# Kernel tuning notes

Hardware: AMD Instinct MI355X
Metric: run time of the kernel (lower is better)

Reference implementation:

```python
import jax, jax.numpy as jnp
import numpy as np
from jax import lax

IN_CHANNELS = 4
STEPS_IN_ITR = 3


def one_step_ltm(x, T):
    # x: [B, H, W]; T: [B, 10, H, W] (9 stencil weight planes + bias plane)
    B, H, W = x.shape
    xp = jnp.pad(x, ((0, 0), (1, 1), (1, 1)))
    out = T[:, 9]
    k = 0
    # original ordering: X0..X2 scan row-offset with col-offset 0, X3..X5 col 1, X6..X8 col 2
    for dj in range(3):
        for di in range(3):
            out = out + xp[:, di:di + H, dj:dj + W] * T[:, k]
            k += 1
    return out


def setup_inputs() -> dict:
    key = jax.random.key(0)
    k1, k2, k3 = jax.random.split(key, 3)
    B, Tt, C, H, W = 8, 16, 1, 512, 512
    x = jax.random.uniform(k1, (B, Tt, C, H, W), dtype=jnp.float32)
    # stand-in unet: 3x3 SAME conv, in_channels -> 10
    W_unet = jax.random.normal(k2, (10, IN_CHANNELS, 3, 3), dtype=jnp.float32) * 0.1
    b_unet = jax.random.normal(k3, (10,), dtype=jnp.float32) * 0.1
    return {"x": x, "W_unet": W_unet, "b_unet": b_unet}


def reference(x, W_unet, b_unet):
    B, Tt, C, H, W = x.shape
    x_in = x[:, -IN_CHANNELS:, 0]  # [B, in_channels, H, W]
    T = lax.conv_general_dilated(
        x_in, W_unet, window_strides=(1, 1), padding='SAME',
        dimension_numbers=('NCHW', 'OIHW', 'NCHW')) + b_unet[None, :, None, None]

    xt0 = one_step_ltm(x[:, -1, 0], T)  # stored at t=0 WITHOUT sigmoid (as in original)

    def body(xt, _):
        for _j in range(STEPS_IN_ITR):
            xt = one_step_ltm(xt, T)
            xt = jax.nn.sigmoid(one_step_ltm(xt, T))
        return xt, xt

    _, xs = lax.scan(body, xt0, None, length=Tt - 1)  # [Tt-1, B, H, W]
    seq = jnp.concatenate([xt0[None], xs], axis=0)     # [Tt, B, H, W]
    seq = jnp.transpose(seq, (1, 0, 2, 3))             # [B, Tt, H, W]
    xout = jnp.zeros((B, Tt, C, H, W), dtype=x.dtype).at[:, :, 0].set(seq)
    return xout
```

## Files before the change

kernel.cpp:

```cpp
#include <hip/hip_runtime.h>
#include <hip/hip_fp16.h>
#include <math.h>

#define Bd 8
#define Td 16
#define Hd 512
#define Wd 512
#define HWc (Hd * Wd)
#define NPIX (Bd * HWc)

#define CT  16
#define CR  18
#define CP  20
#define CTH2 256

#define WCR 128
#define WCC 64
#define WH  6
#define WTR 140
#define WTC 76
#define WLP 77
#define WTHR 1024
#define WRPG 11
#define WNG 13

#define FMAMIX_LO(acc, wv, hv) \
    asm("v_fma_mix_f32 %0, %1, %2, %0 op_sel:[0,0,0] op_sel_hi:[0,1,0]" \
        : "+v"(acc) : "v"(wv), "v"(hv))
#define FMAMIX_HI(acc, wv, hv) \
    asm("v_fma_mix_f32 %0, %1, %2, %0 op_sel:[0,1,0] op_sel_hi:[0,1,0]" \
        : "+v"(acc) : "v"(wv), "v"(hv))

__device__ __forceinline__ float hi_half_f32(unsigned h) {
    __half2 hh = *(__half2*)&h;
    return __half2float(__high2half(hh));
}

__global__ __launch_bounds__(CTH2)
void conv_step0_kernel(const float* __restrict__ x,
                       const float* __restrict__ Wu,
                       const float* __restrict__ bu,
                       __half2* __restrict__ T,
                       float* __restrict__ out) {
    __shared__ float sX[4][CR][CP];

    int bx  = blockIdx.x;
    int b   = bx >> 10;
    int rem = bx & 1023;
    int by  = rem >> 5;
    int bc  = rem & 31;
    int i0  = by * CT;
    int j0  = bc * CT;

    const float* xb = x + ((size_t)b * Td + 12) * HWc;
    int tid = threadIdx.x;

    for (int idx = tid; idx < 4 * CR * CR; idx += CTH2) {
        int ch = idx / (CR * CR);
        int r2 = idx - ch * (CR * CR);
        int r  = r2 / CR;
        int c  = r2 - r * CR;
        int gi = i0 + r - 1, gj = j0 + c - 1;
        float v = 0.0f;
        if ((unsigned)gi < (unsigned)Hd && (unsigned)gj < (unsigned)Wd)
            v = xb[(size_t)ch * HWc + gi * Wd + gj];
        sX[ch][r][c] = v;
    }
    __syncthreads();

    int tx = tid & 15;
    int ty = tid >> 4;

    float xf[36];
    #pragma unroll
    for (int ch = 0; ch < 4; ++ch)
        #pragma unroll
        for (int kh = 0; kh < 3; ++kh)
            #pragma unroll
            for (int kw = 0; kw < 3; ++kw)
                xf[(ch * 3 + kh) * 3 + kw] = sX[ch][ty + kh][tx + kw];

    int gi = i0 + ty;
    int gj = j0 + tx;
    size_t pix = (size_t)gi * Wd + gj;
    __half2* Tb = T + (size_t)b * 5 * HWc;

    float o0 = 0.0f;
    float accPrev = 0.0f;
    #pragma unroll
    for (int o = 0; o < 10; ++o) {
        const float* wo = Wu + o * 36;
        float acc = bu[o];
        #pragma unroll
        for (int z = 0; z < 36; ++z)
            acc += xf[z] * wo[z];

        if (o < 9)
            o0 += xf[(3 * 3 + (o % 3)) * 3 + (o / 3)] * acc;
        else
            o0 += acc;

        if (o & 1) {
            __half2 h = __floats2half2_rn(accPrev, acc);
            *(unsigned*)(Tb + (size_t)(o >> 1) * HWc + pix) = *(unsigned*)&h;
        }
        accPrev = acc;
    }

    out[(size_t)b * Td * HWc + pix] = o0;
}

__global__ __launch_bounds__(WTHR, 2)
void fused6_wide_kernel(const float* __restrict__ xin,
                        const __half2* __restrict__ T,
                        float* __restrict__ xout) {
    __shared__ float sA[WTR * WLP];
    __shared__ float sB[WTR * WLP];

    int tile = blockIdx.x;
    int b  = tile >> 5;
    int tr = (tile >> 3) & 3;
    int tc = tile & 7;
    int ri = tr * WCR - WH;
    int rj = tc * WCC - WH;

    const float* xb = xin + (size_t)b * Td * HWc;
    const __half2* Tb = T + (size_t)b * 5 * HWc;
    float* ob = xout + (size_t)b * Td * HWc;
    int tid = threadIdx.x;

    for (int idx = tid; idx < WTR * WTC; idx += WTHR) {
        int r = idx / WTC, c = idx - r * WTC;
        int gi = ri + r, gj = rj + c;
        float v = 0.0f;
        if ((unsigned)gi < (unsigned)Hd && (unsigned)gj < (unsigned)Wd)
            v = xb[gi * Wd + gj];
        sA[r * WLP + c] = v;
    }
    for (int idx = tid; idx < 2 * WTC; idx += WTHR) {
        int r = (idx < WTC) ? 0 : (WTR - 1);
        int c = (idx < WTC) ? idx : idx - WTC;
        sB[r * WLP + c] = 0.0f;
    }
    for (int idx = tid; idx < 2 * WTR; idx += WTHR) {
        int r = (idx < WTR) ? idx : idx - WTR;
        int c = (idx < WTR) ? 0 : (WTC - 1);
        sB[r * WLP + c] = 0.0f;
    }

    int g  = tid / WTC;
    int c  = tid - g * WTC;
    int rs = 1 + g * WRPG;
    bool colint = (c >= 1) && (c <= WTC - 2);
    bool active = (g < WNG) && colint;
    int  gj     = rj + c;
    bool colin  = (unsigned)gj < (unsigned)Wd;
    bool colcore = (c >= WH) && (c <= WTC - 1 - WH);

    unsigned treg[WRPG][5];
    #pragma unroll
    for (int jj = 0; jj < WRPG; ++jj) {
        int r  = rs + jj;
        int gi = ri + r;
        bool ok = active && (r <= WTR - 2) && ((unsigned)gi < (unsigned)Hd) && colin;
        #pragma unroll
        for (int q = 0; q < 5; ++q) {
            unsigned v = 0u;
            if (ok) v = *(const unsigned*)(Tb + (size_t)q * HWc + gi * Wd + gj);
            treg[jj][q] = v;
        }
    }
    __syncthreads();

    float* cur = sA;
    float* nxt = sB;

    #pragma unroll
    for (int s = 1; s <= 6; ++s) {
        if (active) {
            float w00 = cur[(rs - 1) * WLP + c - 1];
            float w01 = cur[(rs - 1) * WLP + c];
            float w02 = cur[(rs - 1) * WLP + c + 1];
            float w10 = cur[rs * WLP + c - 1];
            float w11 = cur[rs * WLP + c];
            float w12 = cur[rs * WLP + c + 1];
            #pragma unroll
            for (int jj = 0; jj < WRPG; ++jj) {
                int r  = rs + jj;
                int r2 = (r + 1 <= WTR - 1) ? (r + 1) : (WTR - 1);
                float w20 = cur[r2 * WLP + c - 1];
                float w21 = cur[r2 * WLP + c];
                float w22 = cur[r2 * WLP + c + 1];

                unsigned h0 = treg[jj][0], h1 = treg[jj][1], h2 = treg[jj][2],
                         h3 = treg[jj][3], h4 = treg[jj][4];
                float a = hi_half_f32(h4);
                FMAMIX_LO(a, w00, h0);
                FMAMIX_HI(a, w10, h0);
                FMAMIX_LO(a, w20, h1);
                FMAMIX_HI(a, w01, h1);
                FMAMIX_LO(a, w11, h2);
                FMAMIX_HI(a, w21, h2);
                FMAMIX_LO(a, w02, h3);
                FMAMIX_HI(a, w12, h3);
                FMAMIX_LO(a, w22, h4);
                if ((s & 1) == 0) a = 1.0f / (1.0f + __expf(-a));

                int gi = ri + r;
                if (s < 6) {
                    bool rowok = (r <= WTR - 2);
                    bool inimg = ((unsigned)gi < (unsigned)Hd) && colin;
                    if (rowok) nxt[r * WLP + c] = inimg ? a : 0.0f;
                } else {
                    if (colcore && r >= WH && r <= WTR - 1 - WH)
                        ob[gi * Wd + gj] = a;
                }

                w00 = w10; w01 = w11; w02 = w12;
                w10 = w20; w11 = w21; w12 = w22;
            }
        }
        if (s < 6) {
            __syncthreads();
            float* tmp = cur; cur = nxt; nxt = tmp;
        }
    }
}

extern "C" void kernel_launch(void* const* d_in, const int* in_sizes, int n_in,
                              void* d_out, int out_size, void* d_ws, size_t ws_size,
                              hipStream_t stream) {
    const float* x  = (const float*)d_in[0];
    const float* Wu = (const float*)d_in[1];
    const float* bu = (const float*)d_in[2];
    float* out = (float*)d_out;
    __half2* T = (__half2*)d_ws;

    conv_step0_kernel<<<8192, CTH2, 0, stream>>>(x, Wu, bu, T, out);

    for (int t = 1; t < Td; ++t)
        fused6_wide_kernel<<<256, WTHR, 0, stream>>>(out + (size_t)(t - 1) * HWc, T,
                                                     out + (size_t)t * HWc);
}
```

Measured before the change: 484.0 us.

## Store intermediate state as packed fp16 pairs in LDS, two columns per thread

The fused six-step stencil kernel now keeps the evolving state in shared memory as packed half2 pairs instead of fp32. Each thread computes two adjacent columns using fma_mix with op_sel selecting the fp16 halves. Global loads and stores are vectorized to float2/uint2. This halves LDS footprint and LDS reads per output and cuts the per-thread row count to 6. The cost is that the intermediate activations are rounded to fp16 between steps, which reduces accuracy across the chained steps, and edge pairs need partial half stores.

```diff
diff --git a/kernel.cpp b/kernel.cpp
--- a/kernel.cpp
+++ b/kernel.cpp
@@ -19,21 +19,32 @@
 #define WH  6
 #define WTR 140
 #define WTC 76
-#define WLP 77
-#define WTHR 1024
-#define WRPG 11
-#define WNG 13
-
-#define FMAMIX_LO(acc, wv, hv) \
-    asm("v_fma_mix_f32 %0, %1, %2, %0 op_sel:[0,0,0] op_sel_hi:[0,1,0]" \
-        : "+v"(acc) : "v"(wv), "v"(hv))
-#define FMAMIX_HI(acc, wv, hv) \
-    asm("v_fma_mix_f32 %0, %1, %2, %0 op_sel:[0,1,0] op_sel_hi:[0,1,0]" \
-        : "+v"(acc) : "v"(wv), "v"(hv))
+#define NPR 38
+#define LP2 41
+#define FTH 1024
+#define PRPG 6
+#define PNG 26
+
+#define FMIX_LL(acc, xv, tv) \
+    asm("v_fma_mix_f32 %0, %1, %2, %0 op_sel:[0,0,0] op_sel_hi:[1,1,0]" \
+        : "+v"(acc) : "v"(xv), "v"(tv))
+#define FMIX_LH(acc, xv, tv) \
+    asm("v_fma_mix_f32 %0, %1, %2, %0 op_sel:[0,1,0] op_sel_hi:[1,1,0]" \
+        : "+v"(acc) : "v"(xv), "v"(tv))
+#define FMIX_HL(acc, xv, tv) \
+    asm("v_fma_mix_f32 %0, %1, %2, %0 op_sel:[1,0,0] op_sel_hi:[1,1,0]" \
+        : "+v"(acc) : "v"(xv), "v"(tv))
+#define FMIX_HH(acc, xv, tv) \
+    asm("v_fma_mix_f32 %0, %1, %2, %0 op_sel:[1,1,0] op_sel_hi:[1,1,0]" \
+        : "+v"(acc) : "v"(xv), "v"(tv))
 
 __device__ __forceinline__ float hi_half_f32(unsigned h) {
     __half2 hh = *(__half2*)&h;
     return __half2float(__high2half(hh));
+}
+__device__ __forceinline__ unsigned pack2(float a, float b) {
+    __half2 h = __floats2half2_rn(a, b);
+    return *(unsigned*)&h;
 }
 
 __global__ __launch_bounds__(CTH2)
@@ -110,12 +121,12 @@
     out[(size_t)b * Td * HWc + pix] = o0;
 }
 
-__global__ __launch_bounds__(WTHR, 2)
-void fused6_wide_kernel(const float* __restrict__ xin,
-                        const __half2* __restrict__ T,
-                        float* __restrict__ xout) {
-    __shared__ float sA[WTR * WLP];
-    __shared__ float sB[WTR * WLP];
+__global__ __launch_bounds__(FTH, 2)
+void fused6_pk_kernel(const float* __restrict__ xin,
+                      const __half2* __restrict__ T,
+                      float* __restrict__ xout) {
+    __shared__ unsigned sA2[WTR * LP2];
+    __shared__ unsigned sB2[WTR * LP2];
 
     int tile = blockIdx.x;
     int b  = tile >> 5;
@@ -129,100 +140,130 @@
     float* ob = xout + (size_t)b * Td * HWc;
     int tid = threadIdx.x;
 
-    for (int idx = tid; idx < WTR * WTC; idx += WTHR) {
-        int r = idx / WTC, c = idx - r * WTC;
-        int gi = ri + r, gj = rj + c;
-        float v = 0.0f;
-        if ((unsigned)gi < (unsigned)Hd && (unsigned)gj < (unsigned)Wd)
-            v = xb[gi * Wd + gj];
-        sA[r * WLP + c] = v;
-    }
-    for (int idx = tid; idx < 2 * WTC; idx += WTHR) {
-        int r = (idx < WTC) ? 0 : (WTR - 1);
-        int c = (idx < WTC) ? idx : idx - WTC;
-        sB[r * WLP + c] = 0.0f;
-    }
-    for (int idx = tid; idx < 2 * WTR; idx += WTHR) {
+    for (int idx = tid; idx < WTR * NPR; idx += FTH) {
+        int r = idx / NPR, u = idx - r * NPR;
+        int gi = ri + r, gj0 = rj + 2 * u;
+        unsigned v = 0u;
+        if ((unsigned)gi < (unsigned)Hd && (unsigned)gj0 < (unsigned)Wd) {
+            float2 f = *(const float2*)(xb + gi * Wd + gj0);
+            v = pack2(f.x, f.y);
+        }
+        sA2[r * LP2 + u] = v;
+    }
+    for (int idx = tid; idx < 2 * NPR; idx += FTH) {
+        int r = (idx < NPR) ? 0 : (WTR - 1);
+        int u = (idx < NPR) ? idx : idx - NPR;
+        sB2[r * LP2 + u] = 0u;
+    }
+    for (int idx = tid; idx < 2 * WTR; idx += FTH) {
         int r = (idx < WTR) ? idx : idx - WTR;
-        int c = (idx < WTR) ? 0 : (WTC - 1);
-        sB[r * WLP + c] = 0.0f;
-    }
-
-    int g  = tid / WTC;
-    int c  = tid - g * WTC;
-    int rs = 1 + g * WRPG;
-    bool colint = (c >= 1) && (c <= WTC - 2);
-    bool active = (g < WNG) && colint;
-    int  gj     = rj + c;
-    bool colin  = (unsigned)gj < (unsigned)Wd;
-    bool colcore = (c >= WH) && (c <= WTC - 1 - WH);
-
-    unsigned treg[WRPG][5];
-    #pragma unroll
-    for (int jj = 0; jj < WRPG; ++jj) {
+        int u = (idx < WTR) ? 0 : (NPR - 1);
+        sB2[r * LP2 + u] = 0u;
+    }
+
+    int g = tid / NPR;
+    int u = tid - g * NPR;
+    bool active = (g < PNG);
+    int rs = 1 + g * PRPG;
+    int gj0 = rj + 2 * u;
+    bool pairin = (unsigned)gj0 < (unsigned)Wd;
+    int uL = (u == 0) ? 0 : u - 1;
+    int uR = (u == NPR - 1) ? (NPR - 1) : u + 1;
+
+    unsigned tA[PRPG][5], tB[PRPG][5];
+    #pragma unroll
+    for (int jj = 0; jj < PRPG; ++jj) {
         int r  = rs + jj;
         int gi = ri + r;
-        bool ok = active && (r <= WTR - 2) && ((unsigned)gi < (unsigned)Hd) && colin;
+        bool ok = active && (r <= WTR - 2) && ((unsigned)gi < (unsigned)Hd) && pairin;
         #pragma unroll
         for (int q = 0; q < 5; ++q) {
-            unsigned v = 0u;
-            if (ok) v = *(const unsigned*)(Tb + (size_t)q * HWc + gi * Wd + gj);
-            treg[jj][q] = v;
+            uint2 pk; pk.x = 0u; pk.y = 0u;
+            if (ok) pk = *(const uint2*)(Tb + (size_t)q * HWc + gi * Wd + gj0);
+            tA[jj][q] = pk.x;
+            tB[jj][q] = pk.y;
         }
     }
     __syncthreads();
 
-    float* cur = sA;
-    float* nxt = sB;
+    unsigned* cur = sA2;
+    unsigned* nxt = sB2;
 
     #pragma unroll
     for (int s = 1; s <= 6; ++s) {
         if (active) {
-            float w00 = cur[(rs - 1) * WLP + c - 1];
-            float w01 = cur[(rs - 1) * WLP + c];
-            float w02 = cur[(rs - 1) * WLP + c + 1];
-            float w10 = cur[rs * WLP + c - 1];
-            float w11 = cur[rs * WLP + c];
-            float w12 = cur[rs * WLP + c + 1];
+            int base = (rs - 1) * LP2;
+            unsigned Ap = cur[base + uL], Bp = cur[base + u], Cp = cur[base + uR];
+            base += LP2;
+            unsigned Ac = cur[base + uL], Bc = cur[base + u], Cc = cur[base + uR];
             #pragma unroll
-            for (int jj = 0; jj < WRPG; ++jj) {
+            for (int jj = 0; jj < PRPG; ++jj) {
                 int r  = rs + jj;
-                int r2 = (r + 1 <= WTR - 1) ? (r + 1) : (WTR - 1);
-                float w20 = cur[r2 * WLP + c - 1];
-                float w21 = cur[r2 * WLP + c];
-                float w22 = cur[r2 * WLP + c + 1];
-
-                unsigned h0 = treg[jj][0], h1 = treg[jj][1], h2 = treg[jj][2],
-                         h3 = treg[jj][3], h4 = treg[jj][4];
-                float a = hi_half_f32(h4);
-                FMAMIX_LO(a, w00, h0);
-                FMAMIX_HI(a, w10, h0);
-                FMAMIX_LO(a, w20, h1);
-                FMAMIX_HI(a, w01, h1);
-                FMAMIX_LO(a, w11, h2);
-                FMAMIX_HI(a, w21, h2);
-                FMAMIX_LO(a, w02, h3);
-                FMAMIX_HI(a, w12, h3);
-                FMAMIX_LO(a, w22, h4);
-                if ((s & 1) == 0) a = 1.0f / (1.0f + __expf(-a));
+                int rn = (r + 1 <= WTR - 1) ? (r + 1) : (WTR - 1);
+                int bn = rn * LP2;
+                unsigned An = cur[bn + uL], Bn = cur[bn + u], Cn = cur[bn + uR];
+
+                float a0 = hi_half_f32(tA[jj][4]);
+                FMIX_HL(a0, Ap, tA[jj][0]);
+                FMIX_HH(a0, Ac, tA[jj][0]);
+                FMIX_HL(a0, An, tA[jj][1]);
+                FMIX_LH(a0, Bp, tA[jj][1]);
+                FMIX_LL(a0, Bc, tA[jj][2]);
+                FMIX_LH(a0, Bn, tA[jj][2]);
+                FMIX_HL(a0, Bp, tA[jj][3]);
+                FMIX_HH(a0, Bc, tA[jj][3]);
+                FMIX_HL(a0, Bn, tA[jj][4]);
+                float a1 = hi_half_f32(tB[jj][4]);
+                FMIX_LL(a1, Bp, tB[jj][0]);
+                FMIX_LH(a1, Bc, tB[jj][0]);
+                FMIX_LL(a1, Bn, tB[jj][1]);
+                FMIX_HH(a1, Bp, tB[jj][1]);
+                FMIX_HL(a1, Bc, tB[jj][2]);
+                FMIX_HH(a1, Bn, tB[jj][2]);
+                FMIX_LL(a1, Cp, tB[jj][3]);
+                FMIX_LH(a1, Cc, tB[jj][3]);
+                FMIX_LL(a1, Cn, tB[jj][4]);
+
+                if ((s & 1) == 0) {
+                    a0 = 1.0f / (1.0f + __expf(-a0));
+                    a1 = 1.0f / (1.0f + __expf(-a1));
+                }
 
                 int gi = ri + r;
+                bool inimg = ((unsigned)gi < (unsigned)Hd) && pairin;
+                float v0 = inimg ? a0 : 0.0f;
+                float v1 = inimg ? a1 : 0.0f;
+
                 if (s < 6) {
-                    bool rowok = (r <= WTR - 2);
-                    bool inimg = ((unsigned)gi < (unsigned)Hd) && colin;
-                    if (rowok) nxt[r * WLP + c] = inimg ? a : 0.0f;
+                    if (r <= WTR - 2) {
+                        int cell = r * LP2 + u;
+                        if (u >= 1 && u <= NPR - 2) {
+                            nxt[cell] = pack2(v0, v1);
+                        } else if (u == 0) {
+                            __half h1 = __float2half_rn(v1);
+                            ((unsigned short*)nxt)[cell * 2 + 1] =
+                                *(unsigned short*)&h1;
+                        } else {
+                            __half h0 = __float2half_rn(v0);
+                            ((unsigned short*)nxt)[cell * 2] =
+                                *(unsigned short*)&h0;
+                        }
+                    }
                 } else {
-                    if (colcore && r >= WH && r <= WTR - 1 - WH)
-                        ob[gi * Wd + gj] = a;
+                    if (u >= WH / 2 && u <= (WTC - 2 - WH) / 2 &&
+                        r >= WH && r <= WTR - 1 - WH) {
+                        float2 st; st.x = v0; st.y = v1;
+                        *(float2*)(ob + gi * Wd + gj0) = st;
+                    }
                 }
 
-                w00 = w10; w01 = w11; w02 = w12;
-                w10 = w20; w11 = w21; w12 = w22;
+                Ap = Ac; Bp = Bc; Cp = Cc;
+                Ac = An; Bc = Bn; Cc = Cn;
             }
         }
         if (s < 6) {
             __syncthreads();
-            float* tmp = cur; cur = nxt; nxt = tmp;
+            unsigned* tmp = cur; cur = nxt; nxt = tmp;
         }
     }
 }
@@ -239,6 +280,6 @@
     conv_step0_kernel<<<8192, CTH2, 0, stream>>>(x, Wu, bu, T, out);
 
     for (int t = 1; t < Td; ++t)
-        fused6_wide_kernel<<<256, WTHR, 0, stream>>>(out + (size_t)(t - 1) * HWc, T,
-                                                     out + (size_t)t * HWc);
-}
+        fused6_pk_kernel<<<256, FTH, 0, stream>>>(out + (size_t)(t - 1) * HWc, T,
+                                                  out + (size_t)t * HWc);
+}
```

Measured after the change: 492.4 us. About the same (+1.7%).
